# Optimization experiments

Measured on AMD Instinct MI355X. Metric: run time of the kernel, lower is better.

Reference implementation:

```python
import jax, jax.numpy as jnp
import numpy as np

N = 50000
E = 800000
IN_DIM = 256
HID = 64
HEADS = 4
OUT_DIM = 32
NEG_SLOPE = 0.2
EPS = 1e-5


def segment_softmax(logits, seg, num_segments):
    # logits: [E, H]; softmax over edges sharing the same destination node
    m = jax.ops.segment_max(logits, seg, num_segments=num_segments)
    m = jnp.where(jnp.isfinite(m), m, 0.0)
    e = jnp.exp(logits - m[seg])
    s = jax.ops.segment_sum(e, seg, num_segments=num_segments)
    return e / (s[seg] + 1e-16)


def setup_inputs() -> dict:
    key = jax.random.key(0)
    ks = jax.random.split(key, 16)
    d = {}
    d['x'] = jax.random.normal(ks[0], (N, IN_DIM), dtype=jnp.float32)
    d['edge_index'] = jax.random.randint(ks[1], (2, E), 0, N, dtype=jnp.int64)
    sc = lambda fan: 1.0 / np.sqrt(fan)
    # input transform: Linear(256->128), Linear(128->64)
    d['t1_w'] = jax.random.normal(ks[2], (IN_DIM, IN_DIM // 2), dtype=jnp.float32) * sc(IN_DIM)
    d['t1_b'] = jnp.zeros((IN_DIM // 2,), jnp.float32)
    d['t2_w'] = jax.random.normal(ks[3], (IN_DIM // 2, IN_DIM // 4), dtype=jnp.float32) * sc(IN_DIM // 2)
    d['t2_b'] = jnp.zeros((IN_DIM // 4,), jnp.float32)
    d['g1_w'] = jax.random.normal(ks[4], (IN_DIM // 4, HEADS * HID), dtype=jnp.float32) * sc(IN_DIM // 4)
    d['g1_att_src'] = jax.random.normal(ks[5], (HEADS, HID), dtype=jnp.float32) * sc(HID)
    d['g1_att_dst'] = jax.random.normal(ks[6], (HEADS, HID), dtype=jnp.float32) * sc(HID)
    d['g1_b'] = jnp.zeros((HEADS * HID,), jnp.float32)
    # GraphNorm(256)
    d['gn_w'] = jnp.ones((HEADS * HID,), jnp.float32)
    d['gn_b'] = jnp.zeros((HEADS * HID,), jnp.float32)
    d['gn_ms'] = jnp.ones((HEADS * HID,), jnp.float32)
    # GATConv 2: 256 -> 32, 1 head, no concat (mean == identity for 1 head)
    d['g2_w'] = jax.random.normal(ks[7], (HEADS * HID, OUT_DIM), dtype=jnp.float32) * sc(HEADS * HID)
    d['g2_att_src'] = jax.random.normal(ks[8], (1, OUT_DIM), dtype=jnp.float32) * sc(OUT_DIM)
    d['g2_att_dst'] = jax.random.normal(ks[9], (1, OUT_DIM), dtype=jnp.float32) * sc(OUT_DIM)
    d['g2_b'] = jnp.zeros((OUT_DIM,), jnp.float32)
    return d


def gat_conv(x, src, dst, w, att_src, att_dst, bias, n_nodes):
    heads, ch = att_src.shape
    h = (x @ w).reshape(n_nodes, heads, ch)            # [N,H,C]
    a_src = jnp.sum(h * att_src, axis=-1)              # [N,H]
    a_dst = jnp.sum(h * att_dst, axis=-1)              # [N,H]
    logits = jax.nn.leaky_relu(a_src[src] + a_dst[dst], NEG_SLOPE)  # [E,H]
    alpha = segment_softmax(logits, dst, n_nodes)      # [E,H]
    msgs = alpha[:, :, None] * h[src]                  # [E,H,C]
    out = jax.ops.segment_sum(msgs, dst, num_segments=n_nodes)  # [N,H,C]
    return out.reshape(n_nodes, heads * ch) + bias


def reference(x, edge_index, t1_w, t1_b, t2_w, t2_b,
              g1_w, g1_att_src, g1_att_dst, g1_b,
              gn_w, gn_b, gn_ms,
              g2_w, g2_att_src, g2_att_dst, g2_b):
    src, dst = edge_index[0], edge_index[1]
    # input transform (dropout inactive in eval)
    h = jax.nn.relu(x @ t1_w + t1_b)
    h = jax.nn.relu(h @ t2_w + t2_b)
    # GAT layer 1 (concat heads)
    h = gat_conv(h, src, dst, g1_w, g1_att_src, g1_att_dst, g1_b, N)
    # GraphNorm over the whole graph (batch=None -> single graph)
    mean = jnp.mean(h, axis=0)
    o = h - mean * gn_ms
    var = jnp.mean(o * o, axis=0)
    h = o / jnp.sqrt(var + EPS) * gn_w + gn_b
    h = jax.nn.elu(h)
    # GAT layer 2 (1 head, concat=False)
    h = gat_conv(h, src, dst, g2_w, g2_att_src, g2_att_dst, g2_b, N)
    return jax.nn.log_softmax(h, axis=1)
```

## Files before the change

### kernel.cpp

```cpp
#include <hip/hip_runtime.h>

#define NSLOPE 0.2f
#define GEPS 1e-5f

typedef unsigned short ushortT;
typedef __attribute__((ext_vector_type(8))) unsigned short us8;
typedef __attribute__((ext_vector_type(8))) __bf16 bf16x8;
typedef __attribute__((ext_vector_type(4))) float f32x4;

__device__ __forceinline__ float lrelu(float x) { return x >= 0.f ? x : NSLOPE * x; }
__device__ __forceinline__ ushortT f2bf(float f) {
    unsigned int u = __float_as_uint(f);
    return (ushortT)((u + 0x7fffu + ((u >> 16) & 1u)) >> 16);
}
__device__ __forceinline__ float bf2f(ushortT h) {
    return __uint_as_float((unsigned int)h << 16);
}

__global__ __launch_bounds__(256) void k_prep(
    const float* __restrict__ w1, const float* __restrict__ w2,
    const float* __restrict__ g1w, const float* __restrict__ g2w,
    ushortT* __restrict__ w1t, ushortT* __restrict__ w2t,
    ushortT* __restrict__ g1t, ushortT* __restrict__ g2t)
{
    const int i = blockIdx.x * 256 + threadIdx.x;
    if (i < 128 * 256) { const int c = i >> 8, k = i & 255; w1t[i] = f2bf(w1[k * 128 + c]); }
    if (i < 64 * 128)  { const int c = i >> 7, k = i & 127; w2t[i] = f2bf(w2[k * 64 + c]); }
    if (i < 256 * 64)  { const int c = i >> 6, k = i & 63;  g1t[i] = f2bf(g1w[k * 256 + c]); }
    if (i < 32 * 256)  { const int c = i >> 8, k = i & 255; g2t[i] = f2bf(g2w[k * 32 + c]); }
}

__global__ __launch_bounds__(256) void k_lin1(const float* __restrict__ x,
    const ushortT* __restrict__ w1t, const float* __restrict__ b1,
    ushortT* __restrict__ h1, int n)
{
    __shared__ us8 Ab[64 * 128 / 16];
    __shared__ us8 Bb[128 * 128 / 16];
    char* A = (char*)Ab; char* B = (char*)Bb;
    const int t = threadIdx.x;
    const int w = t >> 6, l = t & 63;
    const int lo = l & 15, hi = l >> 4;
    const int n0 = blockIdx.x * 64;
    const int wm = (w >> 1) * 32, wn = (w & 1) * 64;
    f32x4 acc[2][4];
    #pragma unroll
    for (int mf = 0; mf < 2; ++mf)
        #pragma unroll
        for (int nf = 0; nf < 4; ++nf) acc[mf][nf] = (f32x4){0.f, 0.f, 0.f, 0.f};

    const int arow = t >> 2, ak0 = (t & 3) * 16;
    int agn = n0 + arow; if (agn >= n) agn = n - 1;
    const int asw = (arow & 7) << 4;

    for (int kc = 0; kc < 4; ++kc) {
        __syncthreads();
        {
            ushortT tmp[16];
            const float* xp = &x[(size_t)agn * 256 + kc * 64 + ak0];
            #pragma unroll
            for (int j = 0; j < 4; ++j) {
                const float4 v = *(const float4*)(xp + j * 4);
                tmp[j*4+0] = f2bf(v.x); tmp[j*4+1] = f2bf(v.y);
                tmp[j*4+2] = f2bf(v.z); tmp[j*4+3] = f2bf(v.w);
            }
            *(us8*)(A + arow * 128 + ((ak0 * 2) ^ asw)) = *(us8*)tmp;
            *(us8*)(A + arow * 128 + ((ak0 * 2 + 16) ^ asw)) = *(us8*)(tmp + 8);
        }
        #pragma unroll
        for (int i = 0; i < 4; ++i) {
            const int idx = i * 256 + t, br = idx >> 3, bs = idx & 7;
            const us8 v = *(const us8*)&w1t[(size_t)br * 256 + kc * 64 + bs * 8];
            *(us8*)(B + br * 128 + ((bs * 16) ^ ((br & 7) << 4))) = v;
        }
        __syncthreads();
        #pragma unroll
        for (int ks = 0; ks < 2; ++ks) {
            const int koff = ks * 64 + hi * 16;
            bf16x8 af[2], bf[4];
            #pragma unroll
            for (int mf = 0; mf < 2; ++mf) {
                const int r = wm + mf * 16 + lo;
                af[mf] = *(const bf16x8*)(A + r * 128 + (koff ^ ((r & 7) << 4)));
            }
            #pragma unroll
            for (int nf = 0; nf < 4; ++nf) {
                const int r = wn + nf * 16 + lo;
                bf[nf] = *(const bf16x8*)(B + r * 128 + (koff ^ ((r & 7) << 4)));
            }
            #pragma unroll
            for (int mf = 0; mf < 2; ++mf)
                #pragma unroll
                for (int nf = 0; nf < 4; ++nf)
                    acc[mf][nf] = __builtin_amdgcn_mfma_f32_16x16x32_bf16(af[mf], bf[nf], acc[mf][nf], 0, 0, 0);
        }
    }
    #pragma unroll
    for (int nf = 0; nf < 4; ++nf) {
        const int col = wn + nf * 16 + lo;
        const float bb = b1[col];
        #pragma unroll
        for (int mf = 0; mf < 2; ++mf)
            #pragma unroll
            for (int j = 0; j < 4; ++j) {
                const int r = n0 + wm + mf * 16 + hi * 4 + j;
                if (r < n) h1[(size_t)r * 128 + col] = f2bf(fmaxf(acc[mf][nf][j] + bb, 0.f));
            }
    }
}

__global__ __launch_bounds__(256) void k_lin2(const ushortT* __restrict__ h1,
    const ushortT* __restrict__ w2t, const float* __restrict__ b2,
    ushortT* __restrict__ h2, int n)
{
    __shared__ us8 Ab[64 * 128 / 16];
    __shared__ us8 Bb[64 * 128 / 16];
    char* A = (char*)Ab; char* B = (char*)Bb;
    const int t = threadIdx.x;
    const int w = t >> 6, l = t & 63;
    const int lo = l & 15, hi = l >> 4;
    const int n0 = blockIdx.x * 64;
    const int wm = (w >> 1) * 32, wn = (w & 1) * 32;
    f32x4 acc[2][2];
    #pragma unroll
    for (int mf = 0; mf < 2; ++mf)
        #pragma unroll
        for (int nf = 0; nf < 2; ++nf) acc[mf][nf] = (f32x4){0.f, 0.f, 0.f, 0.f};

    const int arow = t >> 2, ak0 = (t & 3) * 16;
    int agn = n0 + arow; if (agn >= n) agn = n - 1;
    const int asw = (arow & 7) << 4;

    for (int kc = 0; kc < 2; ++kc) {
        __syncthreads();
        {
            const us8 v0 = *(const us8*)&h1[(size_t)agn * 128 + kc * 64 + ak0];
            const us8 v1 = *(const us8*)&h1[(size_t)agn * 128 + kc * 64 + ak0 + 8];
            *(us8*)(A + arow * 128 + ((ak0 * 2) ^ asw)) = v0;
            *(us8*)(A + arow * 128 + ((ak0 * 2 + 16) ^ asw)) = v1;
        }
        #pragma unroll
        for (int i = 0; i < 2; ++i) {
            const int idx = i * 256 + t, br = idx >> 3, bs = idx & 7;
            const us8 v = *(const us8*)&w2t[(size_t)br * 128 + kc * 64 + bs * 8];
            *(us8*)(B + br * 128 + ((bs * 16) ^ ((br & 7) << 4))) = v;
        }
        __syncthreads();
        #pragma unroll
        for (int ks = 0; ks < 2; ++ks) {
            const int koff = ks * 64 + hi * 16;
            bf16x8 af[2], bf[2];
            #pragma unroll
            for (int mf = 0; mf < 2; ++mf) {
                const int r = wm + mf * 16 + lo;
                af[mf] = *(const bf16x8*)(A + r * 128 + (koff ^ ((r & 7) << 4)));
            }
            #pragma unroll
            for (int nf = 0; nf < 2; ++nf) {
                const int r = wn + nf * 16 + lo;
                bf[nf] = *(const bf16x8*)(B + r * 128 + (koff ^ ((r & 7) << 4)));
            }
            #pragma unroll
            for (int mf = 0; mf < 2; ++mf)
                #pragma unroll
                for (int nf = 0; nf < 2; ++nf)
                    acc[mf][nf] = __builtin_amdgcn_mfma_f32_16x16x32_bf16(af[mf], bf[nf], acc[mf][nf], 0, 0, 0);
        }
    }
    #pragma unroll
    for (int nf = 0; nf < 2; ++nf) {
        const int col = wn + nf * 16 + lo;
        const float bb = b2[col];
        #pragma unroll
        for (int mf = 0; mf < 2; ++mf)
            #pragma unroll
            for (int j = 0; j < 4; ++j) {
                const int r = n0 + wm + mf * 16 + hi * 4 + j;
                if (r < n) h2[(size_t)r * 64 + col] = f2bf(fmaxf(acc[mf][nf][j] + bb, 0.f));
            }
    }
}

__global__ __launch_bounds__(256) void k_g1feat(const ushortT* __restrict__ h2,
    const ushortT* __restrict__ g1t, const float* __restrict__ attS, const float* __restrict__ attD,
    ushortT* __restrict__ hg1, float* __restrict__ a1s, float* __restrict__ a1d, int n)
{
    __shared__ us8 Ab[64 * 128 / 16];
    __shared__ us8 Bb[256 * 128 / 16];
    char* A = (char*)Ab; char* B = (char*)Bb;
    const int t = threadIdx.x;
    const int w = t >> 6, l = t & 63;
    const int lo = l & 15, hi = l >> 4;
    const int n0 = blockIdx.x * 64;
    const int wm = (w >> 1) * 32, wn = (w & 1) * 128;
    f32x4 acc[2][8];
    #pragma unroll
    for (int mf = 0; mf < 2; ++mf)
        #pragma unroll
        for (int nf = 0; nf < 8; ++nf) acc[mf][nf] = (f32x4){0.f, 0.f, 0.f, 0.f};

    {
        const int arow = t >> 2, ak0 = (t & 3) * 16;
        int agn = n0 + arow; if (agn >= n) agn = n - 1;
        const int asw = (arow & 7) << 4;
        const us8 v0 = *(const us8*)&h2[(size_t)agn * 64 + ak0];
        const us8 v1 = *(const us8*)&h2[(size_t)agn * 64 + ak0 + 8];
        *(us8*)(A + arow * 128 + ((ak0 * 2) ^ asw)) = v0;
        *(us8*)(A + arow * 128 + ((ak0 * 2 + 16) ^ asw)) = v1;
    }
    #pragma unroll
    for (int i = 0; i < 8; ++i) {
        const int idx = i * 256 + t, br = idx >> 3, bs = idx & 7;
        const us8 v = *(const us8*)&g1t[(size_t)br * 64 + bs * 8];
        *(us8*)(B + br * 128 + ((bs * 16) ^ ((br & 7) << 4))) = v;
    }
    __syncthreads();
    #pragma unroll
    for (int ks = 0; ks < 2; ++ks) {
        const int koff = ks * 64 + hi * 16;
        bf16x8 af[2];
        #pragma unroll
        for (int mf = 0; mf < 2; ++mf) {
            const int r = wm + mf * 16 + lo;
            af[mf] = *(const bf16x8*)(A + r * 128 + (koff ^ ((r & 7) << 4)));
        }
        #pragma unroll
        for (int nf = 0; nf < 8; ++nf) {
            const int r = wn + nf * 16 + lo;
            const bf16x8 bf = *(const bf16x8*)(B + r * 128 + (koff ^ ((r & 7) << 4)));
            #pragma unroll
            for (int mf = 0; mf < 2; ++mf)
                acc[mf][nf] = __builtin_amdgcn_mfma_f32_16x16x32_bf16(af[mf], bf, acc[mf][nf], 0, 0, 0);
        }
    }
    float sS[8], sD[8];
    #pragma unroll
    for (int nf = 0; nf < 8; ++nf) {
        sS[nf] = attS[wn + nf * 16 + lo];
        sD[nf] = attD[wn + nf * 16 + lo];
    }
    const int hA = wn >> 6, hB = hA + 1;
    #pragma unroll
    for (int mf = 0; mf < 2; ++mf)
        #pragma unroll
        for (int j = 0; j < 4; ++j) {
            const int r = n0 + wm + mf * 16 + hi * 4 + j;
            float pSA = 0.f, pDA = 0.f, pSB = 0.f, pDB = 0.f;
            #pragma unroll
            for (int nf = 0; nf < 4; ++nf) {
                pSA = fmaf(acc[mf][nf][j], sS[nf], pSA);
                pDA = fmaf(acc[mf][nf][j], sD[nf], pDA);
                pSB = fmaf(acc[mf][nf + 4][j], sS[nf + 4], pSB);
                pDB = fmaf(acc[mf][nf + 4][j], sD[nf + 4], pDB);
            }
            #pragma unroll
            for (int off = 1; off < 16; off <<= 1) {
                pSA += __shfl_xor(pSA, off);
                pDA += __shfl_xor(pDA, off);
                pSB += __shfl_xor(pSB, off);
                pDB += __shfl_xor(pDB, off);
            }
            if (r < n) {
                if (lo == 0) {
                    a1s[r * 4 + hA] = pSA; a1s[r * 4 + hB] = pSB;
                    a1d[r * 4 + hA] = pDA; a1d[r * 4 + hB] = pDB;
                }
                #pragma unroll
                for (int nf = 0; nf < 8; ++nf)
                    hg1[(size_t)r * 256 + wn + nf * 16 + lo] = f2bf(acc[mf][nf][j]);
            }
        }
}

__global__ __launch_bounds__(256) void k_g2feat(const ushortT* __restrict__ out1,
    const float* __restrict__ cscale, const float* __restrict__ cshift,
    const ushortT* __restrict__ g2t, const float* __restrict__ attS, const float* __restrict__ attD,
    ushortT* __restrict__ hg2, float* __restrict__ a2s, float* __restrict__ a2d, int n)
{
    __shared__ us8 Ab[64 * 128 / 16];
    __shared__ us8 Bb[32 * 128 / 16];
    char* A = (char*)Ab; char* B = (char*)Bb;
    const int t = threadIdx.x;
    const int w = t >> 6, l = t & 63;
    const int lo = l & 15, hi = l >> 4;
    const int n0 = blockIdx.x * 64;
    const int wm = w * 16;
    f32x4 acc[2];
    acc[0] = (f32x4){0.f, 0.f, 0.f, 0.f};
    acc[1] = (f32x4){0.f, 0.f, 0.f, 0.f};

    const int arow = t >> 2, ak0 = (t & 3) * 16;
    int agn = n0 + arow; if (agn >= n) agn = n - 1;
    const int asw = (arow & 7) << 4;

    for (int kc = 0; kc < 4; ++kc) {
        __syncthreads();
        {
            ushortT tmp[16];
            const us8 v0 = *(const us8*)&out1[(size_t)agn * 256 + kc * 64 + ak0];
            const us8 v1 = *(const us8*)&out1[(size_t)agn * 256 + kc * 64 + ak0 + 8];
            #pragma unroll
            for (int j = 0; j < 8; ++j) {
                float a = bf2f(v0[j]) * cscale[kc * 64 + ak0 + j] + cshift[kc * 64 + ak0 + j];
                float b = bf2f(v1[j]) * cscale[kc * 64 + ak0 + 8 + j] + cshift[kc * 64 + ak0 + 8 + j];
                a = a > 0.f ? a : __expf(a) - 1.f;
                b = b > 0.f ? b : __expf(b) - 1.f;
                tmp[j] = f2bf(a); tmp[8 + j] = f2bf(b);
            }
            *(us8*)(A + arow * 128 + ((ak0 * 2) ^ asw)) = *(us8*)tmp;
            *(us8*)(A + arow * 128 + ((ak0 * 2 + 16) ^ asw)) = *(us8*)(tmp + 8);
        }
        {
            const int br = t >> 3, bs = t & 7;
            const us8 v = *(const us8*)&g2t[(size_t)br * 256 + kc * 64 + bs * 8];
            *(us8*)(B + br * 128 + ((bs * 16) ^ ((br & 7) << 4))) = v;
        }
        __syncthreads();
        #pragma unroll
        for (int ks = 0; ks < 2; ++ks) {
            const int koff = ks * 64 + hi * 16;
            const int ra = wm + lo;
            const bf16x8 af = *(const bf16x8*)(A + ra * 128 + (koff ^ ((ra & 7) << 4)));
            #pragma unroll
            for (int nf = 0; nf < 2; ++nf) {
                const int r = nf * 16 + lo;
                const bf16x8 bf = *(const bf16x8*)(B + r * 128 + (koff ^ ((r & 7) << 4)));
                acc[nf] = __builtin_amdgcn_mfma_f32_16x16x32_bf16(af, bf, acc[nf], 0, 0, 0);
            }
        }
    }
    float sS[2], sD[2];
    sS[0] = attS[lo]; sS[1] = attS[16 + lo];
    sD[0] = attD[lo]; sD[1] = attD[16 + lo];
    #pragma unroll
    for (int j = 0; j < 4; ++j) {
        const int r = n0 + wm + hi * 4 + j;
        float pS = fmaf(acc[0][j], sS[0], acc[1][j] * sS[1]);
        float pD = fmaf(acc[0][j], sD[0], acc[1][j] * sD[1]);
        #pragma unroll
        for (int off = 1; off < 16; off <<= 1) {
            pS += __shfl_xor(pS, off);
            pD += __shfl_xor(pD, off);
        }
        if (r < n) {
            if (lo == 0) { a2s[r] = pS; a2d[r] = pD; }
            hg2[(size_t)r * 32 + lo] = f2bf(acc[0][j]);
            hg2[(size_t)r * 32 + 16 + lo] = f2bf(acc[1][j]);
        }
    }
}

__global__ void k_hist(const int* __restrict__ dst, int* __restrict__ deg, int e) {
    int i = blockIdx.x * 256 + threadIdx.x;
    if (i < e) atomicAdd(&deg[dst[i]], 1);
}

__global__ __launch_bounds__(256) void k_scan1(const int* __restrict__ deg, int* __restrict__ offs,
                                               int* __restrict__ bsum, int n)
{
    __shared__ int sm[256];
    const int t = threadIdx.x;
    const int i = blockIdx.x * 256 + t;
    const int v = (i < n) ? deg[i] : 0;
    sm[t] = v;
    __syncthreads();
    for (int off = 1; off < 256; off <<= 1) {
        int add = (t >= off) ? sm[t - off] : 0;
        __syncthreads();
        sm[t] += add;
        __syncthreads();
    }
    if (i < n) offs[i] = sm[t] - v;
    if (t == 255) bsum[blockIdx.x] = sm[255];
}

__global__ __launch_bounds__(256) void k_scan2(int* __restrict__ bsum, int nb) {
    __shared__ int sm[256];
    const int t = threadIdx.x;
    const int v = (t < nb) ? bsum[t] : 0;
    sm[t] = v;
    __syncthreads();
    for (int off = 1; off < 256; off <<= 1) {
        int add = (t >= off) ? sm[t - off] : 0;
        __syncthreads();
        sm[t] += add;
        __syncthreads();
    }
    if (t < nb) bsum[t] = sm[t] - v;
}

__global__ void k_scan3(int* __restrict__ offs, int* __restrict__ cursor,
                        const int* __restrict__ bsum, int n, int e) {
    int i = blockIdx.x * 256 + threadIdx.x;
    if (i < n) {
        int o = offs[i] + bsum[i >> 8];
        offs[i] = o;
        cursor[i] = o;
    }
    if (i == 0) offs[n] = e;
}

__global__ void k_scatter(const int* __restrict__ src, const int* __restrict__ dst,
                          int* __restrict__ cursor, int* __restrict__ csr, int e) {
    int i = blockIdx.x * 256 + threadIdx.x;
    if (i < e) {
        int p = atomicAdd(&cursor[dst[i]], 1);
        csr[p] = src[i];
    }
}

__global__ __launch_bounds__(256) void k_alpha1(
    const float* __restrict__ a1s, const float* __restrict__ a1d,
    const int* __restrict__ offs, const int* __restrict__ csr,
    float* __restrict__ alphaE, int n)
{
    const int l = threadIdx.x & 15;
    const int d = blockIdx.x * 16 + (threadIdx.x >> 4);
    if (d >= n) return;
    const int start = offs[d], end = offs[d + 1];
    const float4* __restrict__ a1s4 = (const float4*)a1s;
    const float4 adv = ((const float4*)a1d)[d];
    const float ad0 = adv.x, ad1 = adv.y, ad2 = adv.z, ad3 = adv.w;

    float m0 = -1e30f, m1 = -1e30f, m2 = -1e30f, m3 = -1e30f;
    float s0 = 0.f, s1 = 0.f, s2 = 0.f, s3 = 0.f;
    for (int e = start + l; e < end; e += 16) {
        const float4 av = a1s4[csr[e]];
        const float l0 = lrelu(av.x + ad0), l1 = lrelu(av.y + ad1);
        const float l2 = lrelu(av.z + ad2), l3 = lrelu(av.w + ad3);
        float nm;
        nm = fmaxf(m0, l0); s0 = s0 * __expf(m0 - nm) + __expf(l0 - nm); m0 = nm;
        nm = fmaxf(m1, l1); s1 = s1 * __expf(m1 - nm) + __expf(l1 - nm); m1 = nm;
        nm = fmaxf(m2, l2); s2 = s2 * __expf(m2 - nm) + __expf(l2 - nm); m2 = nm;
        nm = fmaxf(m3, l3); s3 = s3 * __expf(m3 - nm) + __expf(l3 - nm); m3 = nm;
    }
    for (int off = 1; off < 16; off <<= 1) {
        float om, os, nm;
        om = __shfl_xor(m0, off, 16); os = __shfl_xor(s0, off, 16);
        nm = fmaxf(m0, om); s0 = s0 * __expf(m0 - nm) + os * __expf(om - nm); m0 = nm;
        om = __shfl_xor(m1, off, 16); os = __shfl_xor(s1, off, 16);
        nm = fmaxf(m1, om); s1 = s1 * __expf(m1 - nm) + os * __expf(om - nm); m1 = nm;
        om = __shfl_xor(m2, off, 16); os = __shfl_xor(s2, off, 16);
        nm = fmaxf(m2, om); s2 = s2 * __expf(m2 - nm) + os * __expf(om - nm); m2 = nm;
        om = __shfl_xor(m3, off, 16); os = __shfl_xor(s3, off, 16);
        nm = fmaxf(m3, om); s3 = s3 * __expf(m3 - nm) + os * __expf(om - nm); m3 = nm;
    }
    const float i0 = 1.f / (s0 + 1e-16f), i1 = 1.f / (s1 + 1e-16f);
    const float i2 = 1.f / (s2 + 1e-16f), i3 = 1.f / (s3 + 1e-16f);
    for (int e = start + l; e < end; e += 16) {
        const float4 av = a1s4[csr[e]];
        float4 o;
        o.x = __expf(lrelu(av.x + ad0) - m0) * i0;
        o.y = __expf(lrelu(av.y + ad1) - m1) * i1;
        o.z = __expf(lrelu(av.z + ad2) - m2) * i2;
        o.w = __expf(lrelu(av.w + ad3) - m3) * i3;
        *(float4*)&alphaE[(size_t)e * 4] = o;
    }
}

__global__ __launch_bounds__(256, 8) void k_pv1(
    const ushortT* __restrict__ hg1, const float* __restrict__ alphaE,
    const int* __restrict__ offs, const int* __restrict__ csr,
    const float* __restrict__ bias, ushortT* __restrict__ out1, int n)
{
    const int lane = threadIdx.x & 63;
    const int d = blockIdx.x * 4 + (threadIdx.x >> 6);
    if (d >= n) return;
    const int start = offs[d], end = offs[d + 1];
    const int cg = lane & 31;
    const int c = cg * 8;
    const int es = lane >> 5;
    const int head = cg >> 3;
    float acc[8];
    #pragma unroll
    for (int j = 0; j < 8; ++j) acc[j] = 0.f;

    #pragma unroll 4
    for (int e = start + es; e < end; e += 2) {
        const int si = csr[e];
        const float al = alphaE[(size_t)e * 4 + head];
        const us8 hv = *(const us8*)&hg1[(size_t)si * 256 + c];
        #pragma unroll
        for (int j = 0; j < 8; ++j) acc[j] = fmaf(al, bf2f(hv[j]), acc[j]);
    }
    #pragma unroll
    for (int j = 0; j < 8; ++j) acc[j] += __shfl_xor(acc[j], 32);
    if (es == 0) {
        const float4 b0 = *(const float4*)&bias[c];
        const float4 b1 = *(const float4*)&bias[c + 4];
        us8 o;
        o[0] = f2bf(acc[0] + b0.x); o[1] = f2bf(acc[1] + b0.y);
        o[2] = f2bf(acc[2] + b0.z); o[3] = f2bf(acc[3] + b0.w);
        o[4] = f2bf(acc[4] + b1.x); o[5] = f2bf(acc[5] + b1.y);
        o[6] = f2bf(acc[6] + b1.z); o[7] = f2bf(acc[7] + b1.w);
        *(us8*)&out1[(size_t)d * 256 + c] = o;
    }
}

__global__ __launch_bounds__(256) void k_colstat(const ushortT* __restrict__ out1,
    float* __restrict__ colsum, float* __restrict__ colsq, int n)
{
    const int t = threadIdx.x;
    float s = 0.f, q = 0.f;
    for (int r = blockIdx.x; r < n; r += gridDim.x) {
        const float v = bf2f(out1[(size_t)r * 256 + t]);
        s += v;
        q += v * v;
    }
    atomicAdd(&colsum[t], s);
    atomicAdd(&colsq[t], q);
}

__global__ void k_norm_params(const float* __restrict__ colsum, const float* __restrict__ colsq,
    const float* __restrict__ gw, const float* __restrict__ gb, const float* __restrict__ gms,
    float* __restrict__ scale, float* __restrict__ shift, int n)
{
    const int t = threadIdx.x;
    const float invn = 1.f / (float)n;
    const float mean = colsum[t] * invn;
    const float msq = colsq[t] * invn;
    const float ms = gms[t];
    const float var = msq - 2.f * ms * mean * mean + ms * ms * mean * mean;
    const float sc = gw[t] * rsqrtf(var + GEPS);
    scale[t] = sc;
    shift[t] = gb[t] - mean * ms * sc;
}

__global__ __launch_bounds__(256) void k_alpha2(
    const float* __restrict__ a2s, const float* __restrict__ a2d,
    const int* __restrict__ offs, const int* __restrict__ csr,
    float* __restrict__ alphaE2, int n)
{
    const int l = threadIdx.x & 15;
    const int d = blockIdx.x * 16 + (threadIdx.x >> 4);
    if (d >= n) return;
    const int start = offs[d], end = offs[d + 1];
    const float adv = a2d[d];
    float m = -1e30f, s = 0.f;
    for (int e = start + l; e < end; e += 16) {
        const float lv = lrelu(a2s[csr[e]] + adv);
        const float nm = fmaxf(m, lv);
        s = s * __expf(m - nm) + __expf(lv - nm);
        m = nm;
    }
    for (int off = 1; off < 16; off <<= 1) {
        const float om = __shfl_xor(m, off, 16), os = __shfl_xor(s, off, 16);
        const float nm = fmaxf(m, om);
        s = s * __expf(m - nm) + os * __expf(om - nm);
        m = nm;
    }
    const float inv = 1.f / (s + 1e-16f);
    for (int e = start + l; e < end; e += 16)
        alphaE2[e] = __expf(lrelu(a2s[csr[e]] + adv) - m) * inv;
}

__global__ __launch_bounds__(256, 8) void k_pv2(
    const ushortT* __restrict__ hg2, const float* __restrict__ alphaE2,
    const int* __restrict__ offs, const int* __restrict__ csr,
    const float* __restrict__ bias, float* __restrict__ out, int n)
{
    const int l = threadIdx.x & 15;
    const int d = blockIdx.x * 16 + (threadIdx.x >> 4);
    if (d >= n) return;
    const int start = offs[d], end = offs[d + 1];
    const int c = l * 2;
    float acc0 = 0.f, acc1 = 0.f;
    #pragma unroll 8
    for (int e = start; e < end; ++e) {
        const int si = csr[e];
        const float al = alphaE2[e];
        const ushort2 hv = *(const ushort2*)&hg2[(size_t)si * 32 + c];
        acc0 = fmaf(al, bf2f(hv.x), acc0);
        acc1 = fmaf(al, bf2f(hv.y), acc1);
    }
    const float v0 = acc0 + bias[c];
    const float v1 = acc1 + bias[c + 1];
    float mx = fmaxf(v0, v1);
    for (int off = 1; off < 16; off <<= 1) mx = fmaxf(mx, __shfl_xor(mx, off, 16));
    float se = __expf(v0 - mx) + __expf(v1 - mx);
    for (int off = 1; off < 16; off <<= 1) se += __shfl_xor(se, off, 16);
    const float ls = __logf(se);
    float2 o = {v0 - mx - ls, v1 - mx - ls};
    *(float2*)&out[(size_t)d * 32 + c] = o;
}

extern "C" void kernel_launch(void* const* d_in, const int* in_sizes, int n_in,
                              void* d_out, int out_size, void* d_ws, size_t ws_size,
                              hipStream_t stream)
{
    const float* x    = (const float*)d_in[0];
    const int*   ei   = (const int*)d_in[1];
    const float* t1w  = (const float*)d_in[2];
    const float* t1b  = (const float*)d_in[3];
    const float* t2w  = (const float*)d_in[4];
    const float* t2b  = (const float*)d_in[5];
    const float* g1w  = (const float*)d_in[6];
    const float* g1as = (const float*)d_in[7];
    const float* g1ad = (const float*)d_in[8];
    const float* g1b  = (const float*)d_in[9];
    const float* gnw  = (const float*)d_in[10];
    const float* gnb  = (const float*)d_in[11];
    const float* gnms = (const float*)d_in[12];
    const float* g2w  = (const float*)d_in[13];
    const float* g2as = (const float*)d_in[14];
    const float* g2ad = (const float*)d_in[15];
    const float* g2b  = (const float*)d_in[16];

    const int N = in_sizes[0] / 256;
    const int E = in_sizes[1] / 2;
    const int* srcA = ei;
    const int* dstA = ei + E;

    char* ws = (char*)d_ws;
    size_t cur = 0;
    auto alloc = [&](size_t bytes) -> char* {
        char* p = ws + cur;
        cur += (bytes + 255) & ~(size_t)255;
        return p;
    };
    ushortT* h1      = (ushortT*)alloc((size_t)N * 128 * 2);
    ushortT* h2      = (ushortT*)alloc((size_t)N * 64 * 2);
    ushortT* hg1     = (ushortT*)alloc((size_t)N * 256 * 2);
    float*   a1s     = (float*)alloc((size_t)N * 4 * 4);
    float*   a1d     = (float*)alloc((size_t)N * 4 * 4);
    ushortT* out1    = (ushortT*)alloc((size_t)N * 256 * 2);
    ushortT* hg2     = (ushortT*)alloc((size_t)N * 32 * 2);
    float*   a2s     = (float*)alloc((size_t)N * 4);
    float*   a2d     = (float*)alloc((size_t)N * 4);
    int*     deg     = (int*)alloc((size_t)(N + 1) * 4);
    int*     offs    = (int*)alloc((size_t)(N + 1) * 4);
    int*     cursor  = (int*)alloc((size_t)N * 4);
    int*     bsum    = (int*)alloc(1024);
    int*     csr     = (int*)alloc((size_t)E * 4);
    float*   alphaE  = (float*)alloc((size_t)E * 4 * 4);
    float*   alphaE2 = (float*)alloc((size_t)E * 4);
    float*   colsum  = (float*)alloc(1024);
    float*   colsq   = (float*)alloc(1024);
    float*   cscale  = (float*)alloc(1024);
    float*   cshift  = (float*)alloc(1024);
    ushortT* w1t     = (ushortT*)alloc(128 * 256 * 2);
    ushortT* w2t     = (ushortT*)alloc(64 * 128 * 2);
    ushortT* g1t     = (ushortT*)alloc(256 * 64 * 2);
    ushortT* g2t     = (ushortT*)alloc(32 * 256 * 2);

    hipMemsetAsync(deg, 0, (size_t)(N + 1) * 4, stream);
    hipMemsetAsync(colsum, 0, 2048, stream);

    const int EB  = (E + 255) / 256;
    const int NB  = (N + 255) / 256;
    const int B64 = (N + 63) / 64;
    const int B16 = (N + 15) / 16;
    const int B4  = (N + 3) / 4;

    k_prep<<<128, 256, 0, stream>>>(t1w, t2w, g1w, g2w, w1t, w2t, g1t, g2t);
    k_lin1<<<B64, 256, 0, stream>>>(x, w1t, t1b, h1, N);
    k_lin2<<<B64, 256, 0, stream>>>(h1, w2t, t2b, h2, N);
    k_g1feat<<<B64, 256, 0, stream>>>(h2, g1t, g1as, g1ad, hg1, a1s, a1d, N);
    k_hist<<<EB, 256, 0, stream>>>(dstA, deg, E);
    k_scan1<<<NB, 256, 0, stream>>>(deg, offs, bsum, N);
    k_scan2<<<1, 256, 0, stream>>>(bsum, NB);
    k_scan3<<<NB, 256, 0, stream>>>(offs, cursor, bsum, N, E);
    k_scatter<<<EB, 256, 0, stream>>>(srcA, dstA, cursor, csr, E);
    k_alpha1<<<B16, 256, 0, stream>>>(a1s, a1d, offs, csr, alphaE, N);
    k_pv1<<<B4, 256, 0, stream>>>(hg1, alphaE, offs, csr, g1b, out1, N);
    k_colstat<<<256, 256, 0, stream>>>(out1, colsum, colsq, N);
    k_norm_params<<<1, 256, 0, stream>>>(colsum, colsq, gnw, gnb, gnms, cscale, cshift, N);
    k_g2feat<<<B64, 256, 0, stream>>>(out1, cscale, cshift, g2t, g2as, g2ad, hg2, a2s, a2d, N);
    k_alpha2<<<B16, 256, 0, stream>>>(a2s, a2d, offs, csr, alphaE2, N);
    k_pv2<<<B16, 256, 0, stream>>>(hg2, alphaE2, offs, csr, g2b, (float*)d_out, N);
}
```

Before: 320.5 us.

## Split hg1 into 32-channel slabs and fuse column stats into aggregation

The GAT1 feature matrix is now stored as eight channel-group slabs of 32 bf16 channels per node. Aggregation blocks are assigned one slab and 64 destination nodes, so the gathered working set per slab (about 3.2 MB) can stay cache-resident. The GraphNorm column sum and sum-of-squares are accumulated inside the aggregation kernel, which removes the separate k_colstat pass over out1. The cost is that each gather is now only 64 bytes per source row, that csr and alpha are reread eight times (once per slab), and that the stats use fp32 values before bf16 rounding.

Result: slower. 347.2 us (+8.3%).

```diff
diff --git a/kernel.cpp b/kernel.cpp
--- a/kernel.cpp
+++ b/kernel.cpp
@@ -182,7 +182,7 @@
 
 __global__ __launch_bounds__(256) void k_g1feat(const ushortT* __restrict__ h2,
     const ushortT* __restrict__ g1t, const float* __restrict__ attS, const float* __restrict__ attD,
-    ushortT* __restrict__ hg1, float* __restrict__ a1s, float* __restrict__ a1d, int n)
+    ushortT* __restrict__ hg1g, float* __restrict__ a1s, float* __restrict__ a1d, int n)
 {
     __shared__ us8 Ab[64 * 128 / 16];
     __shared__ us8 Bb[256 * 128 / 16];
@@ -265,8 +265,10 @@
                     a1d[r * 4 + hA] = pDA; a1d[r * 4 + hB] = pDB;
                 }
                 #pragma unroll
-                for (int nf = 0; nf < 8; ++nf)
-                    hg1[(size_t)r * 256 + wn + nf * 16 + lo] = f2bf(acc[mf][nf][j]);
+                for (int nf = 0; nf < 8; ++nf) {
+                    const int ch = wn + nf * 16 + lo;
+                    hg1g[((size_t)(ch >> 5) * n + r) * 32 + (ch & 31)] = f2bf(acc[mf][nf][j]);
+                }
             }
         }
 }
@@ -458,56 +460,55 @@
 }
 
 __global__ __launch_bounds__(256, 8) void k_pv1(
-    const ushortT* __restrict__ hg1, const float* __restrict__ alphaE,
+    const ushortT* __restrict__ hg1g, const float* __restrict__ alphaE,
     const int* __restrict__ offs, const int* __restrict__ csr,
-    const float* __restrict__ bias, ushortT* __restrict__ out1, int n)
-{
+    const float* __restrict__ bias, ushortT* __restrict__ out1,
+    float* __restrict__ colsum, float* __restrict__ colsq, int n)
+{
+    __shared__ float scs[32], scq[32];
+    const int g = blockIdx.x & 7;
+    const int nb = blockIdx.x >> 3;
+    const int wave = threadIdx.x >> 6;
     const int lane = threadIdx.x & 63;
-    const int d = blockIdx.x * 4 + (threadIdx.x >> 6);
-    if (d >= n) return;
-    const int start = offs[d], end = offs[d + 1];
-    const int cg = lane & 31;
-    const int c = cg * 8;
-    const int es = lane >> 5;
-    const int head = cg >> 3;
-    float acc[8];
-    #pragma unroll
-    for (int j = 0; j < 8; ++j) acc[j] = 0.f;
-
-    #pragma unroll 4
-    for (int e = start + es; e < end; e += 2) {
-        const int si = csr[e];
-        const float al = alphaE[(size_t)e * 4 + head];
-        const us8 hv = *(const us8*)&hg1[(size_t)si * 256 + c];
-        #pragma unroll
-        for (int j = 0; j < 8; ++j) acc[j] = fmaf(al, bf2f(hv[j]), acc[j]);
-    }
-    #pragma unroll
-    for (int j = 0; j < 8; ++j) acc[j] += __shfl_xor(acc[j], 32);
+    const int es = lane >> 4;
+    const int l = lane & 15;
+    const int c = l * 2;
+    const int head = g >> 1;
+    const ushortT* __restrict__ slab = hg1g + (size_t)g * n * 32;
+    if (threadIdx.x < 32) { scs[threadIdx.x] = 0.f; scq[threadIdx.x] = 0.f; }
+    __syncthreads();
+    const float b0 = bias[g * 32 + c], b1 = bias[g * 32 + c + 1];
+    float cs0 = 0.f, cs1 = 0.f, cq0 = 0.f, cq1 = 0.f;
+    const int dEnd = min(n, (nb + 1) * 64);
+    for (int d = nb * 64 + wave; d < dEnd; d += 4) {
+        const int start = offs[d], end = offs[d + 1];
+        float a0 = 0.f, a1 = 0.f;
+        #pragma unroll 4
+        for (int e = start + es; e < end; e += 4) {
+            const int si = csr[e];
+            const float al = alphaE[(size_t)e * 4 + head];
+            const ushort2 hv = *(const ushort2*)&slab[(size_t)si * 32 + c];
+            a0 = fmaf(al, bf2f(hv.x), a0);
+            a1 = fmaf(al, bf2f(hv.y), a1);
+        }
+        a0 += __shfl_xor(a0, 16); a0 += __shfl_xor(a0, 32);
+        a1 += __shfl_xor(a1, 16); a1 += __shfl_xor(a1, 32);
+        if (es == 0) {
+            const float v0 = a0 + b0, v1 = a1 + b1;
+            ushort2 o = {f2bf(v0), f2bf(v1)};
+            *(ushort2*)&out1[(size_t)d * 256 + g * 32 + c] = o;
+            cs0 += v0; cs1 += v1; cq0 += v0 * v0; cq1 += v1 * v1;
+        }
+    }
     if (es == 0) {
-        const float4 b0 = *(const float4*)&bias[c];
-        const float4 b1 = *(const float4*)&bias[c + 4];
-        us8 o;
-        o[0] = f2bf(acc[0] + b0.x); o[1] = f2bf(acc[1] + b0.y);
-        o[2] = f2bf(acc[2] + b0.z); o[3] = f2bf(acc[3] + b0.w);
-        o[4] = f2bf(acc[4] + b1.x); o[5] = f2bf(acc[5] + b1.y);
-        o[6] = f2bf(acc[6] + b1.z); o[7] = f2bf(acc[7] + b1.w);
-        *(us8*)&out1[(size_t)d * 256 + c] = o;
-    }
-}
-
-__global__ __launch_bounds__(256) void k_colstat(const ushortT* __restrict__ out1,
-    float* __restrict__ colsum, float* __restrict__ colsq, int n)
-{
-    const int t = threadIdx.x;
-    float s = 0.f, q = 0.f;
-    for (int r = blockIdx.x; r < n; r += gridDim.x) {
-        const float v = bf2f(out1[(size_t)r * 256 + t]);
-        s += v;
-        q += v * v;
-    }
-    atomicAdd(&colsum[t], s);
-    atomicAdd(&colsq[t], q);
+        atomicAdd(&scs[c], cs0); atomicAdd(&scs[c + 1], cs1);
+        atomicAdd(&scq[c], cq0); atomicAdd(&scq[c + 1], cq1);
+    }
+    __syncthreads();
+    if (threadIdx.x < 32) {
+        atomicAdd(&colsum[g * 32 + threadIdx.x], scs[threadIdx.x]);
+        atomicAdd(&colsq[g * 32 + threadIdx.x], scq[threadIdx.x]);
+    }
 }
 
 __global__ void k_norm_params(const float* __restrict__ colsum, const float* __restrict__ colsq,
@@ -619,7 +620,7 @@
     };
     ushortT* h1      = (ushortT*)alloc((size_t)N * 128 * 2);
     ushortT* h2      = (ushortT*)alloc((size_t)N * 64 * 2);
-    ushortT* hg1     = (ushortT*)alloc((size_t)N * 256 * 2);
+    ushortT* hg1g    = (ushortT*)alloc((size_t)N * 256 * 2);
     float*   a1s     = (float*)alloc((size_t)N * 4 * 4);
     float*   a1d     = (float*)alloc((size_t)N * 4 * 4);
     ushortT* out1    = (ushortT*)alloc((size_t)N * 256 * 2);
@@ -649,20 +650,18 @@
     const int NB  = (N + 255) / 256;
     const int B64 = (N + 63) / 64;
     const int B16 = (N + 15) / 16;
-    const int B4  = (N + 3) / 4;
 
     k_prep<<<128, 256, 0, stream>>>(t1w, t2w, g1w, g2w, w1t, w2t, g1t, g2t);
     k_lin1<<<B64, 256, 0, stream>>>(x, w1t, t1b, h1, N);
     k_lin2<<<B64, 256, 0, stream>>>(h1, w2t, t2b, h2, N);
-    k_g1feat<<<B64, 256, 0, stream>>>(h2, g1t, g1as, g1ad, hg1, a1s, a1d, N);
+    k_g1feat<<<B64, 256, 0, stream>>>(h2, g1t, g1as, g1ad, hg1g, a1s, a1d, N);
     k_hist<<<EB, 256, 0, stream>>>(dstA, deg, E);
     k_scan1<<<NB, 256, 0, stream>>>(deg, offs, bsum, N);
     k_scan2<<<1, 256, 0, stream>>>(bsum, NB);
     k_scan3<<<NB, 256, 0, stream>>>(offs, cursor, bsum, N, E);
     k_scatter<<<EB, 256, 0, stream>>>(srcA, dstA, cursor, csr, E);
     k_alpha1<<<B16, 256, 0, stream>>>(a1s, a1d, offs, csr, alphaE, N);
-    k_pv1<<<B4, 256, 0, stream>>>(hg1, alphaE, offs, csr, g1b, out1, N);
-    k_colstat<<<256, 256, 0, stream>>>(out1, colsum, colsq, N);
+    k_pv1<<<B64 * 8, 256, 0, stream>>>(hg1g, alphaE, offs, csr, g1b, out1, colsum, colsq, N);
     k_norm_params<<<1, 256, 0, stream>>>(colsum, colsq, gnw, gnb, gnms, cscale, cshift, N);
     k_g2feat<<<B64, 256, 0, stream>>>(out1, cscale, cshift, g2t, g2as, g2ad, hg2, a2s, a2d, N);
     k_alpha2<<<B16, 256, 0, stream>>>(a2s, a2d, offs, csr, alphaE2, N);
```
